# Kernel optimization log

Measured on AMD Instinct MI355X. Metric: run time of the kernel, lower is better.

## Reference

```python
import jax, jax.numpy as jnp
import numpy as np

PH = 12        # planning_horizon
B = 16         # batch
H = 256        # belief dim
Z = 64         # state dim
CAND = 512     # candidates
TOPK = 64      # top_candidates
ITERS = 3      # optimisation_iters
NTOOLS = 36    # num_tools
CONT = 2       # cont_action_size (hard-coded in source)
MIN_A, MAX_A = -1.0, 1.0


def setup_inputs() -> dict:
    ks = jax.random.split(jax.random.key(0), 9)
    s = 0.05  # weight scale keeps tanh in its linear-ish regime
    return {
        "belief": jax.random.normal(ks[0], (B, H), jnp.float32),
        "state": jax.random.normal(ks[1], (B, Z), jnp.float32),
        "Wb": jax.random.normal(ks[2], (H, H), jnp.float32) * s,
        "Wa": jax.random.normal(ks[3], (3, H), jnp.float32) * s,
        "bb": jnp.zeros((H,), jnp.float32),
        "Ws": jax.random.normal(ks[4], (H, Z), jnp.float32) * s,
        "bs": jnp.zeros((Z,), jnp.float32),
        "wrb": jax.random.normal(ks[5], (H,), jnp.float32) * s,
        "wrs": jax.random.normal(ks[6], (Z,), jnp.float32) * s,
    }


def reference(belief, state, Wb, Wa, bb, Ws, bs, wrb, wrs):
    # expand to (B*CAND, .) exactly like unsqueeze+expand+reshape (row-repeat)
    b0 = jnp.repeat(belief, CAND, axis=0)  # (B*CAND, H)
    s0 = jnp.repeat(state, CAND, axis=0)   # (B*CAND, Z)

    action_mean = jnp.zeros((PH, B, 1, CONT), jnp.float32)
    action_std = jnp.ones((PH, B, 1, CONT), jnp.float32)
    freq = jnp.ones((PH, B, 1, NTOOLS), jnp.float32)

    key = jax.random.key(42)
    for it in range(ITERS):
        k_disc, k_noise, key = jax.random.split(key, 3)
        # multinomial(freq, CAND, replacement=True) per (PH*B) row
        logits = jnp.log(freq.reshape(-1, NTOOLS))            # (PH*B, NTOOLS)
        disc = jax.random.categorical(k_disc, logits, shape=(CAND, PH * B)).T
        disc = disc.reshape(PH, B * CAND, 1).astype(jnp.float32)
        # continuous: mean + std * N(0,1), clamped
        noise = jax.random.normal(k_noise, (PH, B, CAND, CONT), jnp.float32)
        cont = jnp.clip(action_mean + action_std * noise, MIN_A, MAX_A)
        cont = cont.reshape(PH, B * CAND, CONT)
        actions = jnp.concatenate([disc, cont], axis=-1)       # (PH, B*CAND, 3)

        # rollout: stand-in recurrent transition + linear reward
        def step(carry, a_t):
            b, s_ = carry
            b = jnp.tanh(b @ Wb + a_t @ Wa + bb)
            s_ = jnp.tanh(b @ Ws + bs)
            return (b, s_), (b, s_)

        _, (beliefs, states) = jax.lax.scan(step, (b0, s0), actions)
        returns = (beliefs @ wrb + states @ wrs).sum(axis=0)   # (B*CAND,)

        # top-k candidates per batch element
        _, idx = jax.lax.top_k(returns.reshape(B, CAND), TOPK)  # (B, TOPK)
        actions_r = actions.reshape(PH, B, CAND, 1 + CONT)
        best = jnp.take_along_axis(actions_r, idx[None, :, :, None], axis=2)  # (PH,B,TOPK,3)

        cont_best = best[..., 1:]
        action_mean = cont_best.mean(axis=2, keepdims=True)
        action_std = jnp.std(cont_best, axis=2, keepdims=True)  # unbiased=False

        # batched histogram over TOPK discrete actions (histc with unit bins),
        # +1 smoothing, normalize -- one fused pass instead of PH*B histc calls
        dints = best[..., 0].astype(jnp.int32)                  # (PH, B, TOPK)
        hist = jax.nn.one_hot(dints, NTOOLS, dtype=jnp.float32).sum(axis=2) + 1.0
        freq = (hist / hist.sum(axis=-1, keepdims=True))[:, :, None, :]

    disc_final = jnp.argmax(freq[0, :, 0, :], axis=-1).astype(jnp.float32)[:, None]  # (B,1)
    cont_final = action_mean[0, :, 0, :]                                             # (B,CONT)
    return jnp.concatenate([disc_final, cont_final], axis=1)                         # (B,3)
```

## Files before the change

### kernel.cpp

```cpp
#include <hip/hip_runtime.h>
#include <cstdint>
#include <cmath>

#define PARTITIONABLE 1

constexpr int kPH = 12;
constexpr int kB = 16;
constexpr int kH = 256;
constexpr int kZ = 64;
constexpr int kCand = 512;
constexpr int kTopK = 64;
constexpr int kTools = 36;
constexpr int kRT = kB * kCand;
constexpr uint32_t kDiscTotal = (uint32_t)kCand * kPH * kB * kTools;
constexpr uint32_t kContTotal = (uint32_t)kPH * kB * kCand * 2;

constexpr int kRowsB = 16;

__host__ __device__ inline void tf2x32(uint32_t k0, uint32_t k1,
                                       uint32_t x0, uint32_t x1,
                                       uint32_t& o0, uint32_t& o1) {
  uint32_t ks2 = k0 ^ k1 ^ 0x1BD11BDAu;
  x0 += k0; x1 += k1;
#define TFROT(v, d) (((v) << (d)) | ((v) >> (32 - (d))))
#define TFR(r) { x0 += x1; x1 = TFROT(x1, r); x1 ^= x0; }
  TFR(13) TFR(15) TFR(26) TFR(6)
  x0 += k1;  x1 += ks2 + 1u;
  TFR(17) TFR(29) TFR(16) TFR(24)
  x0 += ks2; x1 += k0 + 2u;
  TFR(13) TFR(15) TFR(26) TFR(6)
  x0 += k0;  x1 += k1 + 3u;
  TFR(17) TFR(29) TFR(16) TFR(24)
  x0 += k1;  x1 += ks2 + 4u;
  TFR(13) TFR(15) TFR(26) TFR(6)
  x0 += ks2; x1 += k0 + 5u;
#undef TFR
#undef TFROT
  o0 = x0; o1 = x1;
}

__device__ inline uint32_t jax_bits32(uint32_t k0, uint32_t k1,
                                      uint32_t idx, uint32_t total) {
#if PARTITIONABLE
  (void)total;
  uint32_t y0, y1;
  tf2x32(k0, k1, 0u, idx, y0, y1);
  return y0 ^ y1;
#else
  uint32_t half = total >> 1;
  uint32_t y0, y1;
  if (idx < half) { tf2x32(k0, k1, idx, idx + half, y0, y1); return y0; }
  else            { tf2x32(k0, k1, idx - half, idx, y0, y1); return y1; }
#endif
}

static void host_split3(uint32_t k0, uint32_t k1, uint32_t out[3][2]) {
#if PARTITIONABLE
  for (uint32_t i = 0; i < 3; ++i)
    tf2x32(k0, k1, 0u, i, out[i][0], out[i][1]);
#else
  uint32_t a0,a1,b0,b1,c0,c1;
  tf2x32(k0, k1, 0u, 3u, a0, a1);
  tf2x32(k0, k1, 1u, 4u, b0, b1);
  tf2x32(k0, k1, 2u, 5u, c0, c1);
  out[0][0]=a0; out[0][1]=b0;
  out[1][0]=c0; out[1][1]=a1;
  out[2][0]=b1; out[2][1]=c1;
#endif
}

__device__ inline float erfinv_xla(float x) {
  float xx = x * x;
  float w = -(float)log1p((double)(-xx));
  float p;
  if (w < 5.0f) {
    float ww = w - 2.5f;
    p = 2.81022636e-08f;
    p = fmaf(p, ww, 3.43273939e-07f);
    p = fmaf(p, ww, -3.5233877e-06f);
    p = fmaf(p, ww, -4.39150654e-06f);
    p = fmaf(p, ww, 0.00021858087f);
    p = fmaf(p, ww, -0.00125372503f);
    p = fmaf(p, ww, -0.00417768164f);
    p = fmaf(p, ww, 0.246640727f);
    p = fmaf(p, ww, 1.50140941f);
  } else {
    float ww = sqrtf(w) - 3.0f;
    p = -0.000200214257f;
    p = fmaf(p, ww, 0.000100950558f);
    p = fmaf(p, ww, 0.00134934322f);
    p = fmaf(p, ww, -0.00367342844f);
    p = fmaf(p, ww, 0.00573950773f);
    p = fmaf(p, ww, -0.0076224613f);
    p = fmaf(p, ww, 0.00943887047f);
    p = fmaf(p, ww, 1.00167406f);
    p = fmaf(p, ww, 2.83297682f);
  }
  return p * x;
}

__global__ __launch_bounds__(256) void k_sample_disc(
    uint32_t kd0, uint32_t kd1, const float* __restrict__ lfreq,
    float* __restrict__ discA, int it0) {
  int gid = blockIdx.x * 256 + threadIdx.x;
  if (gid >= kCand * kPH * kB) return;
  int c = gid / (kPH * kB);
  int j = gid - c * (kPH * kB);
  int best = 0;
  if (it0) {
    uint32_t bm = 0u;
    for (int t = 0; t < kTools; ++t) {
      uint32_t bits = jax_bits32(kd0, kd1, (uint32_t)(gid * kTools + t), kDiscTotal);
      uint32_t m = bits >> 9;
      if (t == 0 || m > bm) { bm = m; best = t; }
    }
  } else {
    const float* lf = lfreq + j * kTools;
    float bv = 0.0f;
    for (int t = 0; t < kTools; ++t) {
      uint32_t bits = jax_bits32(kd0, kd1, (uint32_t)(gid * kTools + t), kDiscTotal);
      float u = __uint_as_float((bits >> 9) | 0x3F800000u) - 1.0f;
      if (u == 0.0f) u = 1.17549435e-38f;
      float l1 = (float)log((double)u);
      float g = -(float)log((double)(-l1));
      float val = g + lf[t];
      if (t == 0 || val > bv) { bv = val; best = t; }
    }
  }
  int ph = j >> 4, b = j & 15;
  discA[ph * kRT + b * kCand + c] = (float)best;
}

__global__ __launch_bounds__(256) void k_sample_cont(
    uint32_t kn0, uint32_t kn1, const float* __restrict__ meanv,
    const float* __restrict__ stdv, float* __restrict__ contA, int it0) {
  int gid = blockIdx.x * 256 + threadIdx.x;
  if (gid >= (int)kContTotal) return;
  uint32_t bits = jax_bits32(kn0, kn1, (uint32_t)gid, kContTotal);
  float f = __uint_as_float((bits >> 9) | 0x3F800000u) - 1.0f;
  const float lo = -0.99999994f;
  float u = fmaxf(lo, f * 2.0f + lo);
  float n = __uint_as_float(0x3FB504F3u) * erfinv_xla(u);
  int d = gid & 1;
  int c = (gid >> 1) & (kCand - 1);
  int rest = gid >> 10;
  int ph = rest >> 4, b = rest & 15;
  float m, s;
  if (it0) { m = 0.0f; s = 1.0f; }
  else {
    m = meanv[rest * 2 + d];
    s = stdv[rest * 2 + d];
  }
  float x = m + s * n;
  x = fminf(fmaxf(x, -1.0f), 1.0f);
  contA[(ph * kRT + b * kCand + c) * 2 + d] = x;
}

__global__ __launch_bounds__(512, 4) void k_rollout(
    const float* __restrict__ belief,
    const float* __restrict__ discA, const float* __restrict__ contA,
    const float* __restrict__ Wb, const float* __restrict__ Wa,
    const float* __restrict__ bbv_, const float* __restrict__ Ws,
    const float* __restrict__ bs_, const float* __restrict__ wrb,
    const float* __restrict__ wrs, float* __restrict__ ret) {
  __shared__ float sBc[kH * kRowsB];
  __shared__ float pT[3][kRowsB][kH];
  __shared__ float sPT[3][kRowsB][kZ];
  __shared__ float sAD[kPH][kRowsB];
  __shared__ float sA0[kPH][kRowsB];
  __shared__ float sA1[kPH][kRowsB];

  const int tid = threadIdx.x;
  const int row0 = blockIdx.x * kRowsB;
  const int batch = row0 >> 9;

  const int w = tid >> 6;
  const int lane = tid & 63;
  const int rowg = w & 1;
  const int ks = w >> 1;
  const int r0 = rowg * 8;
  const int c0 = lane * 4;

  const int sks = tid >> 7;
  const int zg = lane;

  const float4 bb4  = *reinterpret_cast<const float4*>(&bbv_[c0]);
  const float4 wa04 = *reinterpret_cast<const float4*>(&Wa[c0]);
  const float4 wa14 = *reinterpret_cast<const float4*>(&Wa[kH + c0]);
  const float4 wa24 = *reinterpret_cast<const float4*>(&Wa[2 * kH + c0]);
  const float4 wrb4 = *reinterpret_cast<const float4*>(&wrb[c0]);
  const float bsv = bs_[zg], wrsv = wrs[zg];

  if (tid < kH) {
    float v = belief[batch * kH + tid];
    float4 v4 = make_float4(v, v, v, v);
    float* p = &sBc[tid * kRowsB];
    *reinterpret_cast<float4*>(p + 0) = v4;
    *reinterpret_cast<float4*>(p + 4) = v4;
    *reinterpret_cast<float4*>(p + 8) = v4;
    *reinterpret_cast<float4*>(p + 12) = v4;
  }
  for (int i = tid; i < kPH * kRowsB; i += 512) {
    int ph = i >> 4, r = i & 15;
    int gr = row0 + r;
    sAD[ph][r] = discA[ph * kRT + gr];
    sA0[ph][r] = contA[(ph * kRT + gr) * 2 + 0];
    sA1[ph][r] = contA[(ph * kRT + gr) * 2 + 1];
  }

  float rsum[8] = {0,0,0,0,0,0,0,0};
  float ssum[8] = {0,0,0,0,0,0,0,0};
  __syncthreads();

  const float* bKb = sBc + (ks * 64) * kRowsB + r0;
  const float* wB  = Wb + (size_t)(ks * 64) * kH + c0;
  const float* bKs = sBc + (sks * 64) * kRowsB + r0;
  const float* wS  = Ws + (size_t)(sks * 64) * kZ + zg;

  #pragma unroll 1
  for (int ph = 0; ph < kPH; ++ph) {
    float acc[8][4];
    #pragma unroll
    for (int i = 0; i < 8; ++i)
      #pragma unroll
      for (int j = 0; j < 4; ++j) acc[i][j] = 0.0f;

    #pragma unroll 4
    for (int k = 0; k < 64; ++k) {
      float4 b0 = *reinterpret_cast<const float4*>(bKb + k * kRowsB);
      float4 b1 = *reinterpret_cast<const float4*>(bKb + k * kRowsB + 4);
      float4 wv = *reinterpret_cast<const float4*>(wB + (size_t)k * kH);
      float bvr[8] = {b0.x, b0.y, b0.z, b0.w, b1.x, b1.y, b1.z, b1.w};
      #pragma unroll
      for (int i = 0; i < 8; ++i) {
        acc[i][0] = fmaf(bvr[i], wv.x, acc[i][0]);
        acc[i][1] = fmaf(bvr[i], wv.y, acc[i][1]);
        acc[i][2] = fmaf(bvr[i], wv.z, acc[i][2]);
        acc[i][3] = fmaf(bvr[i], wv.w, acc[i][3]);
      }
    }
    if (ks != 0) {
      #pragma unroll
      for (int i = 0; i < 8; ++i)
        *reinterpret_cast<float4*>(&pT[ks - 1][r0 + i][c0]) =
            make_float4(acc[i][0], acc[i][1], acc[i][2], acc[i][3]);
    }
    __syncthreads();

    if (ks == 0) {
      #pragma unroll
      for (int i = 0; i < 8; ++i) {
        int r = r0 + i;
        float4 p0 = *reinterpret_cast<const float4*>(&pT[0][r][c0]);
        float4 p1 = *reinterpret_cast<const float4*>(&pT[1][r][c0]);
        float4 p2 = *reinterpret_cast<const float4*>(&pT[2][r][c0]);
        float aD = sAD[ph][r], a0 = sA0[ph][r], a1 = sA1[ph][r];
        float t0 = ((acc[i][0] + p0.x) + p1.x) + p2.x + bb4.x
                   + aD * wa04.x + a0 * wa14.x + a1 * wa24.x;
        float t1 = ((acc[i][1] + p0.y) + p1.y) + p2.y + bb4.y
                   + aD * wa04.y + a0 * wa14.y + a1 * wa24.y;
        float t2 = ((acc[i][2] + p0.z) + p1.z) + p2.z + bb4.z
                   + aD * wa04.z + a0 * wa14.z + a1 * wa24.z;
        float t3 = ((acc[i][3] + p0.w) + p1.w) + p2.w + bb4.w
                   + aD * wa04.w + a0 * wa14.w + a1 * wa24.w;
        float n0 = tanhf(t0), n1 = tanhf(t1), n2 = tanhf(t2), n3 = tanhf(t3);
        acc[i][0] = n0; acc[i][1] = n1; acc[i][2] = n2; acc[i][3] = n3;
        rsum[i] = fmaf(n0, wrb4.x, rsum[i]);
        rsum[i] = fmaf(n1, wrb4.y, rsum[i]);
        rsum[i] = fmaf(n2, wrb4.z, rsum[i]);
        rsum[i] = fmaf(n3, wrb4.w, rsum[i]);
      }
      #pragma unroll
      for (int j = 0; j < 4; ++j) {
        float* p = &sBc[(c0 + j) * kRowsB + r0];
        *reinterpret_cast<float4*>(p) =
            make_float4(acc[0][j], acc[1][j], acc[2][j], acc[3][j]);
        *reinterpret_cast<float4*>(p + 4) =
            make_float4(acc[4][j], acc[5][j], acc[6][j], acc[7][j]);
      }
    }
    __syncthreads();

    float sa[8] = {0,0,0,0,0,0,0,0};
    #pragma unroll 4
    for (int k = 0; k < 64; ++k) {
      float4 b0 = *reinterpret_cast<const float4*>(bKs + k * kRowsB);
      float4 b1 = *reinterpret_cast<const float4*>(bKs + k * kRowsB + 4);
      float wv = wS[(size_t)k * kZ];
      sa[0] = fmaf(b0.x, wv, sa[0]);
      sa[1] = fmaf(b0.y, wv, sa[1]);
      sa[2] = fmaf(b0.z, wv, sa[2]);
      sa[3] = fmaf(b0.w, wv, sa[3]);
      sa[4] = fmaf(b1.x, wv, sa[4]);
      sa[5] = fmaf(b1.y, wv, sa[5]);
      sa[6] = fmaf(b1.z, wv, sa[6]);
      sa[7] = fmaf(b1.w, wv, sa[7]);
    }
    if (sks != 0) {
      #pragma unroll
      for (int i = 0; i < 8; ++i) sPT[sks - 1][r0 + i][zg] = sa[i];
    }
    __syncthreads();

    if (sks == 0) {
      #pragma unroll
      for (int i = 0; i < 8; ++i) {
        int r = r0 + i;
        float t = ((sa[i] + sPT[0][r][zg]) + sPT[1][r][zg]) + sPT[2][r][zg] + bsv;
        float sv = tanhf(t);
        ssum[i] = fmaf(sv, wrsv, ssum[i]);
      }
    }
  }

  if (tid < 128) {
    #pragma unroll
    for (int i = 0; i < 8; ++i) {
      float v = rsum[i] + ssum[i];
      v += __shfl_xor(v, 1, 64);
      v += __shfl_xor(v, 2, 64);
      v += __shfl_xor(v, 4, 64);
      v += __shfl_xor(v, 8, 64);
      v += __shfl_xor(v, 16, 64);
      v += __shfl_xor(v, 32, 64);
      if (lane == 0) ret[row0 + r0 + i] = v;
    }
  }
}

__global__ __launch_bounds__(256) void k_topk_stats(
    const float* __restrict__ ret, const float* __restrict__ discA,
    const float* __restrict__ contA, float* __restrict__ freq,
    float* __restrict__ lfreq, float* __restrict__ meanv,
    float* __restrict__ stdv) {
  __shared__ float rv[kCand];
  __shared__ int selc[kTopK];
  __shared__ int hist[kTools];
  const int b = blockIdx.x, tid = threadIdx.x;
  for (int i = tid; i < kCand; i += 256) rv[i] = ret[b * kCand + i];
  __syncthreads();
  for (int c = tid; c < kCand; c += 256) {
    float v = rv[c];
    int rank = 0;
    for (int o = 0; o < kCand; ++o) {
      float vo = rv[o];
      rank += ((vo > v) || (vo == v && o < c)) ? 1 : 0;
    }
    if (rank < kTopK) selc[rank] = c;
  }
  __syncthreads();
  for (int ph = 0; ph < kPH; ++ph) {
    if (tid < kTools) hist[tid] = 0;
    __syncthreads();
    if (tid < kTopK) {
      int c = selc[tid];
      int idx = ph * kRT + b * kCand + c;
      int d = (int)discA[idx];
      atomicAdd(&hist[d], 1);
      float c0 = contA[idx * 2 + 0];
      float c1 = contA[idx * 2 + 1];
      float s0 = c0, s1 = c1;
      #pragma unroll
      for (int sh = 1; sh < 64; sh <<= 1) {
        s0 += __shfl_xor(s0, sh, 64);
        s1 += __shfl_xor(s1, sh, 64);
      }
      float m0 = s0 * (1.0f / 64.0f);
      float m1 = s1 * (1.0f / 64.0f);
      float d0 = c0 - m0, d1 = c1 - m1;
      float q0 = d0 * d0, q1 = d1 * d1;
      #pragma unroll
      for (int sh = 1; sh < 64; sh <<= 1) {
        q0 += __shfl_xor(q0, sh, 64);
        q1 += __shfl_xor(q1, sh, 64);
      }
      if (tid == 0) {
        int o = (ph * kB + b) * 2;
        meanv[o + 0] = m0;
        meanv[o + 1] = m1;
        stdv[o + 0] = sqrtf(q0 * (1.0f / 64.0f));
        stdv[o + 1] = sqrtf(q1 * (1.0f / 64.0f));
      }
    }
    __syncthreads();
    if (tid < kTools) {
      float fq = (float)(hist[tid] + 1) / 100.0f;
      int o = (ph * kB + b) * kTools + tid;
      freq[o] = fq;
      lfreq[o] = (float)log((double)fq);
    }
    __syncthreads();
  }
}

__global__ void k_final(const float* __restrict__ freq,
                        const float* __restrict__ meanv,
                        float* __restrict__ out) {
  int b = threadIdx.x;
  if (b < kB) {
    const float* f = freq + b * kTools;
    int best = 0; float bv = f[0];
    for (int t = 1; t < kTools; ++t)
      if (f[t] > bv) { bv = f[t]; best = t; }
    out[b * 3 + 0] = (float)best;
    out[b * 3 + 1] = meanv[b * 2 + 0];
    out[b * 3 + 2] = meanv[b * 2 + 1];
  }
}

extern "C" void kernel_launch(void* const* d_in, const int* in_sizes, int n_in,
                              void* d_out, int out_size, void* d_ws, size_t ws_size,
                              hipStream_t stream) {
  (void)in_sizes; (void)n_in; (void)out_size; (void)ws_size;
  const float* belief = (const float*)d_in[0];
  const float* Wb  = (const float*)d_in[2];
  const float* Wa  = (const float*)d_in[3];
  const float* bb  = (const float*)d_in[4];
  const float* Ws  = (const float*)d_in[5];
  const float* bs  = (const float*)d_in[6];
  const float* wrb = (const float*)d_in[7];
  const float* wrs = (const float*)d_in[8];
  float* out = (float*)d_out;

  float* w = (float*)d_ws;
  float* discA = w;
  float* contA = discA + kPH * kRT;
  float* ret   = contA + kPH * kRT * 2;
  float* freq  = ret + kRT;
  float* lfreq = freq + kPH * kB * kTools;
  float* meanv = lfreq + kPH * kB * kTools;
  float* stdv  = meanv + kPH * kB * 2;

  uint32_t key0 = 0u, key1 = 42u;
  for (int it = 0; it < 3; ++it) {
    uint32_t ks[3][2];
    host_split3(key0, key1, ks);
    int it0 = (it == 0) ? 1 : 0;
    k_sample_disc<<<dim3((kCand * kPH * kB + 255) / 256), dim3(256), 0, stream>>>(
        ks[0][0], ks[0][1], lfreq, discA, it0);
    k_sample_cont<<<dim3((kContTotal + 255) / 256), dim3(256), 0, stream>>>(
        ks[1][0], ks[1][1], meanv, stdv, contA, it0);
    k_rollout<<<dim3(kRT / kRowsB), dim3(512), 0, stream>>>(
        belief, discA, contA, Wb, Wa, bb, Ws, bs, wrb, wrs, ret);
    k_topk_stats<<<dim3(kB), dim3(256), 0, stream>>>(
        ret, discA, contA, freq, lfreq, meanv, stdv);
    key0 = ks[2][0]; key1 = ks[2][1];
  }
  k_final<<<dim3(1), dim3(64), 0, stream>>>(freq, meanv, out);
}
```

Measured before the change: 1.122 ms.

## Halve rollout rows per block and use tree reduction with distributed tanh

The rollout kernel now handles 8 rows per block with 256 threads, which doubles the grid to 1024 blocks. The K-split partial sums are combined with a two-level pairwise reduction into two shared buffers, and the tanh/reward epilogue is spread across all four waves (2 rows each) instead of one wave doing every row. The belief tile uses a padded stride of 12 to ease bank conflicts. The aim is more parallelism and less serialized epilogue work, at the cost of an extra barrier per phase and twice as many Wb reads per row across blocks.

New measurement: 1.110 ms. No clear change (-1.1%).

```diff
diff --git a/kernel.cpp b/kernel.cpp
--- a/kernel.cpp
+++ b/kernel.cpp
@@ -15,7 +15,8 @@
 constexpr uint32_t kDiscTotal = (uint32_t)kCand * kPH * kB * kTools;
 constexpr uint32_t kContTotal = (uint32_t)kPH * kB * kCand * 2;
 
-constexpr int kRowsB = 16;
+constexpr int kRowsB = 8;
+constexpr int kSB = 12;
 
 __host__ __device__ inline void tf2x32(uint32_t k0, uint32_t k1,
                                        uint32_t x0, uint32_t x1,
@@ -156,16 +157,18 @@
   contA[(ph * kRT + b * kCand + c) * 2 + d] = x;
 }
 
-__global__ __launch_bounds__(512, 4) void k_rollout(
+__global__ __launch_bounds__(256) void k_rollout(
     const float* __restrict__ belief,
     const float* __restrict__ discA, const float* __restrict__ contA,
     const float* __restrict__ Wb, const float* __restrict__ Wa,
     const float* __restrict__ bbv_, const float* __restrict__ Ws,
     const float* __restrict__ bs_, const float* __restrict__ wrb,
     const float* __restrict__ wrs, float* __restrict__ ret) {
-  __shared__ float sBc[kH * kRowsB];
-  __shared__ float pT[3][kRowsB][kH];
-  __shared__ float sPT[3][kRowsB][kZ];
+  __shared__ float sBc[kH * kSB];
+  __shared__ float pA[kRowsB][kH];
+  __shared__ float pB[kRowsB][kH];
+  __shared__ float sA_[kRowsB][kZ];
+  __shared__ float sB_[kRowsB][kZ];
   __shared__ float sAD[kPH][kRowsB];
   __shared__ float sA0[kPH][kRowsB];
   __shared__ float sA1[kPH][kRowsB];
@@ -176,46 +179,38 @@
 
   const int w = tid >> 6;
   const int lane = tid & 63;
-  const int rowg = w & 1;
-  const int ks = w >> 1;
-  const int r0 = rowg * 8;
   const int c0 = lane * 4;
-
-  const int sks = tid >> 7;
-  const int zg = lane;
+  const int fr0 = w * 2;
 
   const float4 bb4  = *reinterpret_cast<const float4*>(&bbv_[c0]);
   const float4 wa04 = *reinterpret_cast<const float4*>(&Wa[c0]);
   const float4 wa14 = *reinterpret_cast<const float4*>(&Wa[kH + c0]);
   const float4 wa24 = *reinterpret_cast<const float4*>(&Wa[2 * kH + c0]);
   const float4 wrb4 = *reinterpret_cast<const float4*>(&wrb[c0]);
-  const float bsv = bs_[zg], wrsv = wrs[zg];
-
-  if (tid < kH) {
+  const float bsv = bs_[lane], wrsv = wrs[lane];
+
+  {
     float v = belief[batch * kH + tid];
     float4 v4 = make_float4(v, v, v, v);
-    float* p = &sBc[tid * kRowsB];
+    float* p = &sBc[tid * kSB];
     *reinterpret_cast<float4*>(p + 0) = v4;
     *reinterpret_cast<float4*>(p + 4) = v4;
-    *reinterpret_cast<float4*>(p + 8) = v4;
-    *reinterpret_cast<float4*>(p + 12) = v4;
-  }
-  for (int i = tid; i < kPH * kRowsB; i += 512) {
-    int ph = i >> 4, r = i & 15;
+  }
+  if (tid < kPH * kRowsB) {
+    int ph = tid >> 3, r = tid & 7;
     int gr = row0 + r;
     sAD[ph][r] = discA[ph * kRT + gr];
     sA0[ph][r] = contA[(ph * kRT + gr) * 2 + 0];
     sA1[ph][r] = contA[(ph * kRT + gr) * 2 + 1];
   }
 
-  float rsum[8] = {0,0,0,0,0,0,0,0};
-  float ssum[8] = {0,0,0,0,0,0,0,0};
+  float rsum[2] = {0.0f, 0.0f};
+  float ssum[2] = {0.0f, 0.0f};
   __syncthreads();
 
-  const float* bKb = sBc + (ks * 64) * kRowsB + r0;
-  const float* wB  = Wb + (size_t)(ks * 64) * kH + c0;
-  const float* bKs = sBc + (sks * 64) * kRowsB + r0;
-  const float* wS  = Ws + (size_t)(sks * 64) * kZ + zg;
+  const float* bKb = sBc + (w * 64) * kSB;
+  const float* wB  = Wb + (size_t)(w * 64) * kH + c0;
+  const float* wS  = Ws + (size_t)(w * 64) * kZ + lane;
 
   #pragma unroll 1
   for (int ph = 0; ph < kPH; ++ph) {
@@ -227,8 +222,8 @@
 
     #pragma unroll 4
     for (int k = 0; k < 64; ++k) {
-      float4 b0 = *reinterpret_cast<const float4*>(bKb + k * kRowsB);
-      float4 b1 = *reinterpret_cast<const float4*>(bKb + k * kRowsB + 4);
+      float4 b0 = *reinterpret_cast<const float4*>(bKb + k * kSB);
+      float4 b1 = *reinterpret_cast<const float4*>(bKb + k * kSB + 4);
       float4 wv = *reinterpret_cast<const float4*>(wB + (size_t)k * kH);
       float bvr[8] = {b0.x, b0.y, b0.z, b0.w, b1.x, b1.y, b1.z, b1.w};
       #pragma unroll
@@ -239,53 +234,67 @@
         acc[i][3] = fmaf(bvr[i], wv.w, acc[i][3]);
       }
     }
-    if (ks != 0) {
+    if (w == 2) {
       #pragma unroll
       for (int i = 0; i < 8; ++i)
-        *reinterpret_cast<float4*>(&pT[ks - 1][r0 + i][c0]) =
+        *reinterpret_cast<float4*>(&pA[i][c0]) =
             make_float4(acc[i][0], acc[i][1], acc[i][2], acc[i][3]);
-    }
-    __syncthreads();
-
-    if (ks == 0) {
+    } else if (w == 3) {
+      #pragma unroll
+      for (int i = 0; i < 8; ++i)
+        *reinterpret_cast<float4*>(&pB[i][c0]) =
+            make_float4(acc[i][0], acc[i][1], acc[i][2], acc[i][3]);
+    }
+    __syncthreads();
+    if (w == 1) {
       #pragma unroll
       for (int i = 0; i < 8; ++i) {
-        int r = r0 + i;
-        float4 p0 = *reinterpret_cast<const float4*>(&pT[0][r][c0]);
-        float4 p1 = *reinterpret_cast<const float4*>(&pT[1][r][c0]);
-        float4 p2 = *reinterpret_cast<const float4*>(&pT[2][r][c0]);
-        float aD = sAD[ph][r], a0 = sA0[ph][r], a1 = sA1[ph][r];
-        float t0 = ((acc[i][0] + p0.x) + p1.x) + p2.x + bb4.x
-                   + aD * wa04.x + a0 * wa14.x + a1 * wa24.x;
-        float t1 = ((acc[i][1] + p0.y) + p1.y) + p2.y + bb4.y
-                   + aD * wa04.y + a0 * wa14.y + a1 * wa24.y;
-        float t2 = ((acc[i][2] + p0.z) + p1.z) + p2.z + bb4.z
-                   + aD * wa04.z + a0 * wa14.z + a1 * wa24.z;
-        float t3 = ((acc[i][3] + p0.w) + p1.w) + p2.w + bb4.w
-                   + aD * wa04.w + a0 * wa14.w + a1 * wa24.w;
-        float n0 = tanhf(t0), n1 = tanhf(t1), n2 = tanhf(t2), n3 = tanhf(t3);
-        acc[i][0] = n0; acc[i][1] = n1; acc[i][2] = n2; acc[i][3] = n3;
-        rsum[i] = fmaf(n0, wrb4.x, rsum[i]);
-        rsum[i] = fmaf(n1, wrb4.y, rsum[i]);
-        rsum[i] = fmaf(n2, wrb4.z, rsum[i]);
-        rsum[i] = fmaf(n3, wrb4.w, rsum[i]);
-      }
-      #pragma unroll
-      for (int j = 0; j < 4; ++j) {
-        float* p = &sBc[(c0 + j) * kRowsB + r0];
-        *reinterpret_cast<float4*>(p) =
-            make_float4(acc[0][j], acc[1][j], acc[2][j], acc[3][j]);
-        *reinterpret_cast<float4*>(p + 4) =
-            make_float4(acc[4][j], acc[5][j], acc[6][j], acc[7][j]);
-      }
-    }
+        float4 t = *reinterpret_cast<const float4*>(&pA[i][c0]);
+        *reinterpret_cast<float4*>(&pA[i][c0]) =
+            make_float4(t.x + acc[i][0], t.y + acc[i][1],
+                        t.z + acc[i][2], t.w + acc[i][3]);
+      }
+    } else if (w == 0) {
+      #pragma unroll
+      for (int i = 0; i < 8; ++i) {
+        float4 t = *reinterpret_cast<const float4*>(&pB[i][c0]);
+        *reinterpret_cast<float4*>(&pB[i][c0]) =
+            make_float4(t.x + acc[i][0], t.y + acc[i][1],
+                        t.z + acc[i][2], t.w + acc[i][3]);
+      }
+    }
+    __syncthreads();
+    float bn[2][4];
+    #pragma unroll
+    for (int rr = 0; rr < 2; ++rr) {
+      int r = fr0 + rr;
+      float4 a = *reinterpret_cast<const float4*>(&pA[r][c0]);
+      float4 b = *reinterpret_cast<const float4*>(&pB[r][c0]);
+      float aD = sAD[ph][r], a0 = sA0[ph][r], a1 = sA1[ph][r];
+      float t0 = (a.x + b.x) + bb4.x + aD * wa04.x + a0 * wa14.x + a1 * wa24.x;
+      float t1 = (a.y + b.y) + bb4.y + aD * wa04.y + a0 * wa14.y + a1 * wa24.y;
+      float t2 = (a.z + b.z) + bb4.z + aD * wa04.z + a0 * wa14.z + a1 * wa24.z;
+      float t3 = (a.w + b.w) + bb4.w + aD * wa04.w + a0 * wa14.w + a1 * wa24.w;
+      bn[rr][0] = tanhf(t0);
+      bn[rr][1] = tanhf(t1);
+      bn[rr][2] = tanhf(t2);
+      bn[rr][3] = tanhf(t3);
+      rsum[rr] = fmaf(bn[rr][0], wrb4.x, rsum[rr]);
+      rsum[rr] = fmaf(bn[rr][1], wrb4.y, rsum[rr]);
+      rsum[rr] = fmaf(bn[rr][2], wrb4.z, rsum[rr]);
+      rsum[rr] = fmaf(bn[rr][3], wrb4.w, rsum[rr]);
+    }
+    #pragma unroll
+    for (int j = 0; j < 4; ++j)
+      *reinterpret_cast<float2*>(&sBc[(c0 + j) * kSB + fr0]) =
+          make_float2(bn[0][j], bn[1][j]);
     __syncthreads();
 
     float sa[8] = {0,0,0,0,0,0,0,0};
     #pragma unroll 4
     for (int k = 0; k < 64; ++k) {
-      float4 b0 = *reinterpret_cast<const float4*>(bKs + k * kRowsB);
-      float4 b1 = *reinterpret_cast<const float4*>(bKs + k * kRowsB + 4);
+      float4 b0 = *reinterpret_cast<const float4*>(bKb + k * kSB);
+      float4 b1 = *reinterpret_cast<const float4*>(bKb + k * kSB + 4);
       float wv = wS[(size_t)k * kZ];
       sa[0] = fmaf(b0.x, wv, sa[0]);
       sa[1] = fmaf(b0.y, wv, sa[1]);
@@ -296,35 +305,41 @@
       sa[6] = fmaf(b1.z, wv, sa[6]);
       sa[7] = fmaf(b1.w, wv, sa[7]);
     }
-    if (sks != 0) {
-      #pragma unroll
-      for (int i = 0; i < 8; ++i) sPT[sks - 1][r0 + i][zg] = sa[i];
-    }
-    __syncthreads();
-
-    if (sks == 0) {
-      #pragma unroll
-      for (int i = 0; i < 8; ++i) {
-        int r = r0 + i;
-        float t = ((sa[i] + sPT[0][r][zg]) + sPT[1][r][zg]) + sPT[2][r][zg] + bsv;
-        float sv = tanhf(t);
-        ssum[i] = fmaf(sv, wrsv, ssum[i]);
-      }
-    }
-  }
-
-  if (tid < 128) {
+    if (w == 2) {
+      #pragma unroll
+      for (int i = 0; i < 8; ++i) sA_[i][lane] = sa[i];
+    } else if (w == 3) {
+      #pragma unroll
+      for (int i = 0; i < 8; ++i) sB_[i][lane] = sa[i];
+    }
+    __syncthreads();
+    if (w == 1) {
+      #pragma unroll
+      for (int i = 0; i < 8; ++i) sA_[i][lane] += sa[i];
+    } else if (w == 0) {
+      #pragma unroll
+      for (int i = 0; i < 8; ++i) sB_[i][lane] += sa[i];
+    }
+    __syncthreads();
     #pragma unroll
-    for (int i = 0; i < 8; ++i) {
-      float v = rsum[i] + ssum[i];
-      v += __shfl_xor(v, 1, 64);
-      v += __shfl_xor(v, 2, 64);
-      v += __shfl_xor(v, 4, 64);
-      v += __shfl_xor(v, 8, 64);
-      v += __shfl_xor(v, 16, 64);
-      v += __shfl_xor(v, 32, 64);
-      if (lane == 0) ret[row0 + r0 + i] = v;
-    }
+    for (int rr = 0; rr < 2; ++rr) {
+      int r = fr0 + rr;
+      float t = (sA_[r][lane] + sB_[r][lane]) + bsv;
+      float sv = tanhf(t);
+      ssum[rr] = fmaf(sv, wrsv, ssum[rr]);
+    }
+  }
+
+  #pragma unroll
+  for (int rr = 0; rr < 2; ++rr) {
+    float v = rsum[rr] + ssum[rr];
+    v += __shfl_xor(v, 1, 64);
+    v += __shfl_xor(v, 2, 64);
+    v += __shfl_xor(v, 4, 64);
+    v += __shfl_xor(v, 8, 64);
+    v += __shfl_xor(v, 16, 64);
+    v += __shfl_xor(v, 32, 64);
+    if (lane == 0) ret[row0 + fr0 + rr] = v;
   }
 }
 
@@ -440,7 +455,7 @@
         ks[0][0], ks[0][1], lfreq, discA, it0);
     k_sample_cont<<<dim3((kContTotal + 255) / 256), dim3(256), 0, stream>>>(
         ks[1][0], ks[1][1], meanv, stdv, contA, it0);
-    k_rollout<<<dim3(kRT / kRowsB), dim3(512), 0, stream>>>(
+    k_rollout<<<dim3(kRT / kRowsB), dim3(256), 0, stream>>>(
         belief, discA, contA, Wb, Wa, bb, Ws, bs, wrb, wrs, ret);
     k_topk_stats<<<dim3(kB), dim3(256), 0, stream>>>(
         ret, discA, contA, freq, lfreq, meanv, stdv);
```
